# Kernel tuning notes

Measured on AMD Instinct MI355X. Metric: run time of the kernel, lower is better.

Reference implementation:

```python
import jax, jax.numpy as jnp
import numpy as np

EMBED_DIM = 256
NUM_HEADS = 8
HEAD_DIM = 32
INNER = NUM_HEADS * HEAD_DIM
NEG_SLOPE = 0.2


def setup_inputs() -> dict:
    key = jax.random.key(0)
    ks = jax.random.split(key, 8)
    B, Ns, Nt = 8, 1024, 1024
    src = jax.random.normal(ks[0], (B, Ns, EMBED_DIM), dtype=jnp.float32)
    trg = jax.random.normal(ks[1], (B, Nt, EMBED_DIM), dtype=jnp.float32)
    src_mask = jnp.ones((B, Ns), dtype=bool)
    trg_mask = jax.random.randint(ks[2], (B, Nt), 0, 2).astype(bool)
    # learned params (xavier-ish scale)
    def xavier(k, shape):
        fan_in, fan_out = shape[0], shape[-1]
        lim = (6.0 / (fan_in + fan_out)) ** 0.5
        return jax.random.uniform(k, shape, jnp.float32, -lim, lim)
    W_src = xavier(ks[3], (EMBED_DIM, INNER))
    W_trg = xavier(ks[4], (EMBED_DIM, INNER))  # is_cross_type=True -> independent
    a_src = xavier(ks[5], (NUM_HEADS, HEAD_DIM))
    a_trg = xavier(ks[6], (NUM_HEADS, HEAD_DIM))
    W_out = xavier(ks[7], (INNER, EMBED_DIM))
    return {"src": src, "trg": trg, "src_mask": src_mask, "trg_mask": trg_mask,
            "W_src": W_src, "W_trg": W_trg, "a_src": a_src, "a_trg": a_trg, "W_out": W_out}


def reference(src, trg, src_mask, trg_mask, W_src, W_trg, a_src, a_trg, W_out):
    B, Ns, _ = src.shape
    Nt = trg.shape[1]
    NH, Dh = NUM_HEADS, HEAD_DIM
    src_proj = (src @ W_src).reshape(B, Ns, NH, Dh)  # dropout p=0
    trg_proj = (trg @ W_trg).reshape(B, Nt, NH, Dh)
    score_src = jnp.einsum('bshd,hd->bsh', src_proj, a_src)
    score_trg = jnp.einsum('bthd,hd->bth', trg_proj, a_trg)
    # (B,Ns,NH,1) + (B,1,NH,Nt) -> (B,Ns,NH,Nt)
    scores = score_src[:, :, :, None] + jnp.transpose(score_trg, (0, 2, 1))[:, None, :, :]
    scores = jnp.where(scores >= 0, scores, NEG_SLOPE * scores)  # LeakyReLU
    edge_mask = src_mask[:, :, None, None] & trg_mask[:, None, None, :]
    scores = jnp.where(edge_mask, scores, -jnp.inf)
    attn = jax.nn.softmax(scores, axis=-1)
    attn = jnp.nan_to_num(attn, nan=0.0)
    aggregated = jnp.einsum('bsht,bthd->bshd', attn, trg_proj)
    output = aggregated.reshape(B, Ns, NH * Dh) @ W_out
    return output, jnp.transpose(attn, (0, 2, 1, 3))
```

## Files before the change

### kernel.cpp

```cpp
#include <hip/hip_runtime.h>
#include <hip/hip_bf16.h>
#include <math.h>

#define NB 8
#define NS 1024
#define NT 1024
#define NE 256
#define NHEADS 8
#define DH 32

typedef __attribute__((ext_vector_type(8))) short short8;
typedef __attribute__((ext_vector_type(8))) unsigned short ushort8;
typedef __attribute__((ext_vector_type(4))) float f32x4;

#define O_VT    0u
#define O_AGGB  (4u<<20)
#define O_WTT   (8u<<20)
#define O_WTO   ((8u<<20)+131072u)
#define O_CSRC  ((8u<<20)+262144u)
#define O_CTRG  (O_CSRC+8192u)
#define O_SSRC  (O_CTRG+8192u)
#define O_STRG  (O_SSRC+262144u)
#define O_FLAG  (O_STRG+262144u)

__device__ __forceinline__ unsigned short f2bf(float f) {
    __hip_bfloat16 h = __float2bfloat16(f);
    union { __hip_bfloat16 h; unsigned short u; } c; c.h = h;
    return c.u;
}
__device__ __forceinline__ float bf2f(unsigned short u) {
    union { unsigned u; float f; } x; x.u = ((unsigned)u) << 16;
    return x.f;
}
__device__ __forceinline__ float leaky(float v) {
    return (v >= 0.f) ? v : 0.2f * v;
}

__global__ __launch_bounds__(256) void setup_kernel(
    const unsigned* __restrict__ tmask_dw, const float* __restrict__ Wsrc,
    const float* __restrict__ Wtrg, const float* __restrict__ Wout,
    const float* __restrict__ asrc, const float* __restrict__ atrg,
    float* __restrict__ c_src, float* __restrict__ c_trg,
    unsigned short* __restrict__ Wt_t, unsigned short* __restrict__ Wt_o,
    int* __restrict__ flag) {
    __shared__ __align__(16) char sm[16640];
    const int tid = threadIdx.x;
    const int bid = blockIdx.x;

    if (bid == 0) {
        __shared__ int s_ok;
        if (tid == 0) s_ok = 1;
        __syncthreads();
        for (int i = tid; i < 2048; i += 256)
            if (tmask_dw[i] > 1u) s_ok = 0;
        __syncthreads();
        if (tid == 0) *flag = s_ok;
    } else if (bid <= 2) {
        float* a_sh = (float*)sm;
        const float* W = (bid == 1) ? Wsrc : Wtrg;
        const float* a = (bid == 1) ? asrc : atrg;
        float* c = (bid == 1) ? c_src : c_trg;
        a_sh[tid] = a[tid];
        __syncthreads();
        const int e = tid;
        float ch[8];
#pragma unroll
        for (int h = 0; h < 8; ++h) ch[h] = 0.f;
        for (int i = 0; i < 64; ++i) {
            const float4 wv = *(const float4*)&W[(size_t)e * NE + i * 4];
            const int h = i >> 3, d0 = (i & 7) * 4;
            ch[h] += wv.x * a_sh[h * 32 + d0] + wv.y * a_sh[h * 32 + d0 + 1] +
                     wv.z * a_sh[h * 32 + d0 + 2] + wv.w * a_sh[h * 32 + d0 + 3];
        }
#pragma unroll
        for (int h = 0; h < 8; ++h) c[h * NE + e] = ch[h];
    } else {
        const int q = bid - 3;
        const float* W = (q >> 4) ? Wout : Wtrg;
        unsigned short* Wt = (q >> 4) ? Wt_o : Wt_t;
        const int tl = q & 15;
        const int k0 = (tl >> 2) * 64, n0 = (tl & 3) * 64;
        float* xs = (float*)sm;
#pragma unroll
        for (int it = 0; it < 4; ++it) {
            const int slot = it * 256 + tid;
            const int k = slot >> 4, c4 = slot & 15;
            const float4 v = *(const float4*)&W[(size_t)(k0 + k) * NE + n0 + c4 * 4];
            float* p = &xs[k * 65 + c4 * 4];
            p[0] = v.x; p[1] = v.y; p[2] = v.z; p[3] = v.w;
        }
        __syncthreads();
#pragma unroll
        for (int it = 0; it < 2; ++it) {
            const int slot = it * 256 + tid;
            const int n = slot >> 3, kc = slot & 7;
            ushort8 v;
#pragma unroll
            for (int e = 0; e < 8; ++e)
                v[e] = f2bf(xs[(kc * 8 + e) * 65 + n]);
            *(ushort8*)&Wt[(size_t)(n0 + n) * NE + k0 + kc * 8] = v;
        }
    }
}

__global__ __launch_bounds__(256) void mid_kernel(
    const float* __restrict__ src, const float* __restrict__ trg,
    const float* __restrict__ c_src, const float* __restrict__ c_trg,
    const unsigned short* __restrict__ Wt_t, unsigned short* __restrict__ Vt,
    float* __restrict__ ssrc, float* __restrict__ strg) {
    __shared__ __align__(16) char sm[49152];
    const int tid = threadIdx.x;
    const int bid = blockIdx.x;

    if (bid < 256) {
        unsigned short* As = (unsigned short*)sm;
        unsigned short* ldsT = (unsigned short*)(sm + 32768);
        const int lane = tid & 63, w = tid >> 6;
        const int row0 = (bid >> 1) * 64;
        const int col0 = (bid & 1) * 128;

#pragma unroll
        for (int it = 0; it < 8; ++it) {
            const int gf = it * 256 + tid;
            const int row = gf >> 5, g3 = gf & 31;
            const float4 a = *(const float4*)&trg[(size_t)(row0 + row) * NE + g3 * 8];
            const float4 b = *(const float4*)&trg[(size_t)(row0 + row) * NE + g3 * 8 + 4];
            ushort8 v;
            v[0] = f2bf(a.x); v[1] = f2bf(a.y); v[2] = f2bf(a.z); v[3] = f2bf(a.w);
            v[4] = f2bf(b.x); v[5] = f2bf(b.y); v[6] = f2bf(b.z); v[7] = f2bf(b.w);
            *(ushort8*)&As[row * NE + ((g3 ^ (row & 7)) * 8)] = v;
        }
        __syncthreads();

        const int r = lane & 15, g = lane >> 4;
        short8 af[8];
#pragma unroll
        for (int kk = 0; kk < 8; ++kk)
            af[kk] = *(const short8*)&As[(w * 16 + r) * NE + (((kk * 4 + g) ^ (r & 7)) * 8)];

        f32x4 acc[8];
#pragma unroll
        for (int nt = 0; nt < 8; ++nt) acc[nt] = (f32x4){0.f, 0.f, 0.f, 0.f};
#pragma unroll
        for (int kk = 0; kk < 8; ++kk) {
#pragma unroll
            for (int nt = 0; nt < 8; ++nt) {
                const int col = col0 + nt * 16 + r;
                const short8 bf = *(const short8*)&Wt_t[(size_t)col * NE + kk * 32 + g * 8];
                acc[nt] = __builtin_amdgcn_mfma_f32_16x16x32_bf16(af[kk], bf, acc[nt], 0, 0, 0);
            }
        }
        __syncthreads();

#pragma unroll
        for (int nt = 0; nt < 8; ++nt) {
            const int cl = nt * 16 + r;
            const int sw = (cl & 7) << 3;
#pragma unroll
            for (int j = 0; j < 4; ++j) {
                const int t = w * 16 + g * 4 + j;
                ldsT[cl * 64 + (t ^ sw)] = f2bf(acc[nt][j]);
            }
        }
        __syncthreads();

        const int b = row0 >> 10, t0 = row0 & 1023;
#pragma unroll
        for (int it = 0; it < 4; ++it) {
            const int slot = it * 256 + tid;
            const int cl = slot >> 3, ch = slot & 7;
            const int colg = col0 + cl;
            const int h = colg >> 5, d = colg & 31;
            *(ushort8*)&Vt[(((size_t)(b * 8 + h)) * 32 + d) * 1024 + t0 + ch * 8] =
                *(const ushort8*)&ldsT[cl * 64 + ch * 8];
        }
    } else {
        float* xs = (float*)sm;
        float* cs = (float*)(sm + 32768);
        const int rowg0 = (bid - 256) * 32;
        const bool is_src = rowg0 < NB * NS;
        const float* X = is_src ? (src + (size_t)rowg0 * NE)
                                : (trg + (size_t)(rowg0 - NB * NS) * NE);
        const float* C = is_src ? c_src : c_trg;
        float* S = is_src ? (ssrc + (size_t)rowg0 * NHEADS)
                          : (strg + (size_t)(rowg0 - NB * NS) * NHEADS);

#pragma unroll
        for (int it = 0; it < 8; ++it) {
            const int slot = it * 256 + tid;
            const int row = slot >> 6, c4 = slot & 63;
            *(float4*)&xs[row * NE + c4 * 4] =
                *(const float4*)&X[(size_t)row * NE + c4 * 4];
            cs[slot] = C[slot];
        }
        __syncthreads();

        const int r = tid >> 3, h = tid & 7;
        float s = 0.f;
        for (int e = 0; e < NE; e += 4) {
            const float4 x = *(const float4*)&xs[r * NE + e];
            const float4 c = *(const float4*)&cs[h * NE + e];
            s += x.x * c.x + x.y * c.y + x.z * c.z + x.w * c.w;
        }
        S[(size_t)r * NHEADS + h] = s;
    }
}

__global__ __launch_bounds__(256) void fused_softmax_agg_kernel(
    const float* __restrict__ ssrc, const float* __restrict__ strg,
    const void* __restrict__ smask, const void* __restrict__ tmask,
    const int* __restrict__ flag_p, const unsigned short* __restrict__ Vt,
    float* __restrict__ attn, unsigned short* __restrict__ agg_bf) {
    const int blk = blockIdx.x;
    const int stile = blk & 15;
    const int h = (blk >> 4) & 7;
    const int b = blk >> 7;
    const int tid = threadIdx.x;
    const int lane = tid & 63;
    const int wave = tid >> 6;
    const int flag = *flag_p;

    __shared__ __align__(16) float s_sm[NT];
    __shared__ float s_inv[64];
    __shared__ float s_ss[64];

    for (int t = tid; t < NT; t += 256) {
        const bool mv = flag ? (((const int*)tmask)[b * NT + t] != 0)
                             : (((const unsigned char*)tmask)[b * NT + t] != 0);
        s_sm[t] = mv ? strg[((size_t)b * NT + t) * NHEADS + h] : -1e30f;
    }
    __syncthreads();

    const int r = lane & 15;
    const int g = lane >> 4;
    const int srow = stile * 64 + wave * 16 + r;
    const float ss = ssrc[((size_t)b * NS + srow) * NHEADS + h];
    const bool rowv = flag ? (((const int*)smask)[b * NS + srow] != 0)
                           : (((const unsigned char*)smask)[b * NS + srow] != 0);
    const int sw = (r & 7) << 3;
    const unsigned short* vr0 = Vt + (size_t)(b * NHEADS + h) * 32768 + r * 1024;
    const unsigned short* vr1 = vr0 + 16 * 1024;

    f32x4 acc0 = {0.f, 0.f, 0.f, 0.f};
    f32x4 acc1 = {0.f, 0.f, 0.f, 0.f};
    float sum = 0.f;
#pragma unroll 4
    for (int c = 0; c < 32; ++c) {
        const int tb = c * 32 + g * 8;
        const short8 b0 = *(const short8*)&vr0[tb ^ sw];
        const short8 b1 = *(const short8*)&vr1[tb ^ sw];
        const float4 v0 = *(const float4*)&s_sm[tb];
        const float4 v1 = *(const float4*)&s_sm[tb + 4];
        const float vv[8] = {v0.x, v0.y, v0.z, v0.w, v1.x, v1.y, v1.z, v1.w};
        short8 pa;
#pragma unroll
        for (int e = 0; e < 8; ++e) {
            const float p = __expf(leaky(ss + vv[e]));
            sum += p;
            pa[e] = (short)f2bf(p);
        }
        acc0 = __builtin_amdgcn_mfma_f32_16x16x32_bf16(pa, b0, acc0, 0, 0, 0);
        acc1 = __builtin_amdgcn_mfma_f32_16x16x32_bf16(pa, b1, acc1, 0, 0, 0);
    }

    sum += __shfl_xor(sum, 16);
    sum += __shfl_xor(sum, 32);
    const float inv = (rowv && sum > 0.f) ? 1.f / sum : 0.f;
    if (g == 0) {
        s_inv[wave * 16 + r] = inv;
        s_ss[wave * 16 + r] = ss;
    }
    __syncthreads();

    {
        const int orow = stile * 64 + wave * 16 + g * 4;
        unsigned short* ab = agg_bf + ((size_t)b * NS + orow) * NE + h * DH + r;
#pragma unroll
        for (int j = 0; j < 4; ++j) {
            const float iv = s_inv[wave * 16 + g * 4 + j];
            ab[(size_t)j * NE] = f2bf(acc0[j] * iv);
            ab[(size_t)j * NE + 16] = f2bf(acc1[j] * iv);
        }
    }

    float* wbase = attn + ((size_t)((b * NHEADS + h) * NS) + stile * 64 + wave * 16) * NT;
    const float* ssv = &s_ss[wave * 16];
    const float* invv = &s_inv[wave * 16];
    for (int rr = 0; rr < 16; ++rr) {
        const float ssr = ssv[rr];
        const float ivr = invv[rr];
        float* arow = wbase + (size_t)rr * NT;
#pragma unroll
        for (int q = 0; q < 4; ++q) {
            const int t0 = q * 256 + lane * 4;
            const float4 sm4 = *(const float4*)&s_sm[t0];
            float4 o;
            o.x = __expf(leaky(ssr + sm4.x)) * ivr;
            o.y = __expf(leaky(ssr + sm4.y)) * ivr;
            o.z = __expf(leaky(ssr + sm4.z)) * ivr;
            o.w = __expf(leaky(ssr + sm4.w)) * ivr;
            *(float4*)&arow[t0] = o;
        }
    }
}

__global__ __launch_bounds__(256) void gemm_out_kernel(
    const unsigned short* __restrict__ Xb, const unsigned short* __restrict__ Wt,
    float* __restrict__ Yf) {
    __shared__ __align__(16) unsigned short As[64 * NE];
    const int tid = threadIdx.x;
    const int lane = tid & 63;
    const int w = tid >> 6;
    const int row0 = blockIdx.x * 64;
    const int col0 = blockIdx.y * 128;

#pragma unroll
    for (int it = 0; it < 8; ++it) {
        const int gf = it * 256 + tid;
        const int row = gf >> 5, g3 = gf & 31;
        const ushort8 v = *(const ushort8*)&Xb[(size_t)(row0 + row) * NE + g3 * 8];
        *(ushort8*)&As[row * NE + ((g3 ^ (row & 7)) * 8)] = v;
    }
    __syncthreads();

    const int r = lane & 15, g = lane >> 4;
    short8 af[8];
#pragma unroll
    for (int kk = 0; kk < 8; ++kk)
        af[kk] = *(const short8*)&As[(w * 16 + r) * NE + (((kk * 4 + g) ^ (r & 7)) * 8)];

    f32x4 acc[8];
#pragma unroll
    for (int nt = 0; nt < 8; ++nt) acc[nt] = (f32x4){0.f, 0.f, 0.f, 0.f};
#pragma unroll
    for (int kk = 0; kk < 8; ++kk) {
#pragma unroll
        for (int nt = 0; nt < 8; ++nt) {
            const int col = col0 + nt * 16 + r;
            const short8 bf = *(const short8*)&Wt[(size_t)col * NE + kk * 32 + g * 8];
            acc[nt] = __builtin_amdgcn_mfma_f32_16x16x32_bf16(af[kk], bf, acc[nt], 0, 0, 0);
        }
    }

#pragma unroll
    for (int nt = 0; nt < 8; ++nt) {
        const int col = col0 + nt * 16 + r;
#pragma unroll
        for (int j = 0; j < 4; ++j) {
            const int row = row0 + w * 16 + g * 4 + j;
            Yf[(size_t)row * NE + col] = acc[nt][j];
        }
    }
}

extern "C" void kernel_launch(void* const* d_in, const int* in_sizes, int n_in,
                              void* d_out, int out_size, void* d_ws, size_t ws_size,
                              hipStream_t stream) {
    const float* src   = (const float*)d_in[0];
    const float* trg   = (const float*)d_in[1];
    const void*  smask = d_in[2];
    const void*  tmask = d_in[3];
    const float* Wsrc  = (const float*)d_in[4];
    const float* Wtrg  = (const float*)d_in[5];
    const float* asrc  = (const float*)d_in[6];
    const float* atrg  = (const float*)d_in[7];
    const float* Wout  = (const float*)d_in[8];

    float* out  = (float*)d_out;
    float* attn = out + (size_t)NB * NS * NE;

    char* wsb = (char*)d_ws;
    unsigned short* Vt     = (unsigned short*)(wsb + O_VT);
    unsigned short* agg_bf = (unsigned short*)(wsb + O_AGGB);
    unsigned short* Wt_t   = (unsigned short*)(wsb + O_WTT);
    unsigned short* Wt_o   = (unsigned short*)(wsb + O_WTO);
    float* c_src = (float*)(wsb + O_CSRC);
    float* c_trg = (float*)(wsb + O_CTRG);
    float* ssrc  = (float*)(wsb + O_SSRC);
    float* strg  = (float*)(wsb + O_STRG);
    int*   flag  = (int*)(wsb + O_FLAG);

    setup_kernel<<<35, 256, 0, stream>>>(
        (const unsigned*)tmask, Wsrc, Wtrg, Wout, asrc, atrg,
        c_src, c_trg, Wt_t, Wt_o, flag);

    mid_kernel<<<768, 256, 0, stream>>>(
        src, trg, c_src, c_trg, Wt_t, Vt, ssrc, strg);

    fused_softmax_agg_kernel<<<NB * NHEADS * (NS / 64), 256, 0, stream>>>(
        ssrc, strg, smask, tmask, flag, Vt, attn, agg_bf);

    gemm_out_kernel<<<dim3(128, 2), 256, 0, stream>>>(agg_bf, Wt_o, out);
}
```

Measured before the change: 98.49 us.

## Fuse output projection into softmax-aggregation kernel with all heads per block

Each block now handles a 16-row source tile across all eight heads, with each wave covering two heads. The aggregated tile stays in swizzled shared memory and the W_out GEMM runs in the same kernel. This removes the separate gemm_out launch and the bf16 aggregate round trip through global memory. Softmax exponentials become raw v_exp_f32 on log2e-prescaled scores. In exchange, shared memory grows to about 40KB per block, the grid shrinks to 512 blocks, and each block repeats the W_out reads.

Result: no change. 98.16 us (-0.3%).

```diff
diff --git a/kernel.cpp b/kernel.cpp
--- a/kernel.cpp
+++ b/kernel.cpp
@@ -8,13 +8,13 @@
 #define NE 256
 #define NHEADS 8
 #define DH 32
+#define LOG2E 1.4426950408889634f
 
 typedef __attribute__((ext_vector_type(8))) short short8;
 typedef __attribute__((ext_vector_type(8))) unsigned short ushort8;
 typedef __attribute__((ext_vector_type(4))) float f32x4;
 
 #define O_VT    0u
-#define O_AGGB  (4u<<20)
 #define O_WTT   (8u<<20)
 #define O_WTO   ((8u<<20)+131072u)
 #define O_CSRC  ((8u<<20)+262144u)
@@ -28,12 +28,13 @@
     union { __hip_bfloat16 h; unsigned short u; } c; c.h = h;
     return c.u;
 }
-__device__ __forceinline__ float bf2f(unsigned short u) {
-    union { unsigned u; float f; } x; x.u = ((unsigned)u) << 16;
-    return x.f;
-}
 __device__ __forceinline__ float leaky(float v) {
     return (v >= 0.f) ? v : 0.2f * v;
+}
+__device__ __forceinline__ float exp2_fast(float x) {
+    float r;
+    asm("v_exp_f32 %0, %1" : "=v"(r) : "v"(x));
+    return r;
 }
 
 __global__ __launch_bounds__(256) void setup_kernel(
@@ -206,149 +207,139 @@
     }
 }
 
-__global__ __launch_bounds__(256) void fused_softmax_agg_kernel(
+__global__ __launch_bounds__(256) void fused_kernel(
     const float* __restrict__ ssrc, const float* __restrict__ strg,
     const void* __restrict__ smask, const void* __restrict__ tmask,
     const int* __restrict__ flag_p, const unsigned short* __restrict__ Vt,
-    float* __restrict__ attn, unsigned short* __restrict__ agg_bf) {
+    const unsigned short* __restrict__ Wt_o,
+    float* __restrict__ attn, float* __restrict__ out) {
     const int blk = blockIdx.x;
-    const int stile = blk & 15;
-    const int h = (blk >> 4) & 7;
-    const int b = blk >> 7;
+    const int q = blk & 63;
+    const int b = blk >> 6;
     const int tid = threadIdx.x;
     const int lane = tid & 63;
-    const int wave = tid >> 6;
+    const int w = tid >> 6;
     const int flag = *flag_p;
 
-    __shared__ __align__(16) float s_sm[NT];
-    __shared__ float s_inv[64];
-    __shared__ float s_ss[64];
+    __shared__ __align__(16) float s_sm[8][1024];
+    __shared__ __align__(16) unsigned short agg_sw[16 * 256];
+    __shared__ float s_inv[8][16];
+    __shared__ float s_ssv[8][16];
 
     for (int t = tid; t < NT; t += 256) {
         const bool mv = flag ? (((const int*)tmask)[b * NT + t] != 0)
                              : (((const unsigned char*)tmask)[b * NT + t] != 0);
-        s_sm[t] = mv ? strg[((size_t)b * NT + t) * NHEADS + h] : -1e30f;
+        const float4 s0 = *(const float4*)&strg[((size_t)b * NT + t) * 8];
+        const float4 s1 = *(const float4*)&strg[((size_t)b * NT + t) * 8 + 4];
+        const float sv[8] = {s0.x, s0.y, s0.z, s0.w, s1.x, s1.y, s1.z, s1.w};
+#pragma unroll
+        for (int h = 0; h < 8; ++h)
+            s_sm[h][t] = mv ? sv[h] * LOG2E : -1e30f;
     }
     __syncthreads();
 
     const int r = lane & 15;
     const int g = lane >> 4;
-    const int srow = stile * 64 + wave * 16 + r;
-    const float ss = ssrc[((size_t)b * NS + srow) * NHEADS + h];
+    const int srow = q * 16 + r;
     const bool rowv = flag ? (((const int*)smask)[b * NS + srow] != 0)
                            : (((const unsigned char*)smask)[b * NS + srow] != 0);
     const int sw = (r & 7) << 3;
-    const unsigned short* vr0 = Vt + (size_t)(b * NHEADS + h) * 32768 + r * 1024;
-    const unsigned short* vr1 = vr0 + 16 * 1024;
-
-    f32x4 acc0 = {0.f, 0.f, 0.f, 0.f};
-    f32x4 acc1 = {0.f, 0.f, 0.f, 0.f};
-    float sum = 0.f;
+
+    f32x4 acc0[2], acc1[2];
+
+#pragma unroll
+    for (int hh = 0; hh < 2; ++hh) {
+        const int h = w * 2 + hh;
+        const float ss2 = ssrc[((size_t)b * NS + srow) * NHEADS + h] * LOG2E;
+        const unsigned short* vr0 = Vt + (size_t)(b * 8 + h) * 32768 + r * 1024;
+        const unsigned short* vr1 = vr0 + 16 * 1024;
+        f32x4 a0 = {0.f, 0.f, 0.f, 0.f};
+        f32x4 a1 = {0.f, 0.f, 0.f, 0.f};
+        float sum = 0.f;
 #pragma unroll 4
-    for (int c = 0; c < 32; ++c) {
-        const int tb = c * 32 + g * 8;
-        const short8 b0 = *(const short8*)&vr0[tb ^ sw];
-        const short8 b1 = *(const short8*)&vr1[tb ^ sw];
-        const float4 v0 = *(const float4*)&s_sm[tb];
-        const float4 v1 = *(const float4*)&s_sm[tb + 4];
-        const float vv[8] = {v0.x, v0.y, v0.z, v0.w, v1.x, v1.y, v1.z, v1.w};
-        short8 pa;
-#pragma unroll
-        for (int e = 0; e < 8; ++e) {
-            const float p = __expf(leaky(ss + vv[e]));
-            sum += p;
-            pa[e] = (short)f2bf(p);
-        }
-        acc0 = __builtin_amdgcn_mfma_f32_16x16x32_bf16(pa, b0, acc0, 0, 0, 0);
-        acc1 = __builtin_amdgcn_mfma_f32_16x16x32_bf16(pa, b1, acc1, 0, 0, 0);
-    }
-
-    sum += __shfl_xor(sum, 16);
-    sum += __shfl_xor(sum, 32);
-    const float inv = (rowv && sum > 0.f) ? 1.f / sum : 0.f;
-    if (g == 0) {
-        s_inv[wave * 16 + r] = inv;
-        s_ss[wave * 16 + r] = ss;
+        for (int c = 0; c < 32; ++c) {
+            const int tb = c * 32 + g * 8;
+            const short8 b0 = *(const short8*)&vr0[tb ^ sw];
+            const short8 b1 = *(const short8*)&vr1[tb ^ sw];
+            const float4 v0 = *(const float4*)&s_sm[h][tb];
+            const float4 v1 = *(const float4*)&s_sm[h][tb + 4];
+            const float vv[8] = {v0.x, v0.y, v0.z, v0.w, v1.x, v1.y, v1.z, v1.w};
+            short8 pa;
+#pragma unroll
+            for (int e = 0; e < 8; ++e) {
+                const float p = exp2_fast(leaky(ss2 + vv[e]));
+                sum += p;
+                pa[e] = (short)f2bf(p);
+            }
+            a0 = __builtin_amdgcn_mfma_f32_16x16x32_bf16(pa, b0, a0, 0, 0, 0);
+            a1 = __builtin_amdgcn_mfma_f32_16x16x32_bf16(pa, b1, a1, 0, 0, 0);
+        }
+        sum += __shfl_xor(sum, 16);
+        sum += __shfl_xor(sum, 32);
+        const float inv = (rowv && sum > 0.f) ? 1.f / sum : 0.f;
+        if (g == 0) {
+            s_inv[h][r] = inv;
+            s_ssv[h][r] = ss2;
+        }
+        acc0[hh] = a0;
+        acc1[hh] = a1;
     }
     __syncthreads();
 
-    {
-        const int orow = stile * 64 + wave * 16 + g * 4;
-        unsigned short* ab = agg_bf + ((size_t)b * NS + orow) * NE + h * DH + r;
+#pragma unroll
+    for (int hh = 0; hh < 2; ++hh) {
+        const int h = w * 2 + hh;
 #pragma unroll
         for (int j = 0; j < 4; ++j) {
-            const float iv = s_inv[wave * 16 + g * 4 + j];
-            ab[(size_t)j * NE] = f2bf(acc0[j] * iv);
-            ab[(size_t)j * NE + 16] = f2bf(acc1[j] * iv);
-        }
-    }
-
-    float* wbase = attn + ((size_t)((b * NHEADS + h) * NS) + stile * 64 + wave * 16) * NT;
-    const float* ssv = &s_ss[wave * 16];
-    const float* invv = &s_inv[wave * 16];
-    for (int rr = 0; rr < 16; ++rr) {
-        const float ssr = ssv[rr];
-        const float ivr = invv[rr];
-        float* arow = wbase + (size_t)rr * NT;
-#pragma unroll
-        for (int q = 0; q < 4; ++q) {
-            const int t0 = q * 256 + lane * 4;
-            const float4 sm4 = *(const float4*)&s_sm[t0];
+            const int row = g * 4 + j;
+            const float iv = s_inv[h][row];
+            int col = h * 32 + r;
+            agg_sw[row * 256 + ((((col >> 3) ^ (row & 7)) << 3) | (col & 7))] =
+                f2bf(acc0[hh][j] * iv);
+            col += 16;
+            agg_sw[row * 256 + ((((col >> 3) ^ (row & 7)) << 3) | (col & 7))] =
+                f2bf(acc1[hh][j] * iv);
+        }
+    }
+    __syncthreads();
+
+    f32x4 oacc[4];
+#pragma unroll
+    for (int nt = 0; nt < 4; ++nt) oacc[nt] = (f32x4){0.f, 0.f, 0.f, 0.f};
+#pragma unroll
+    for (int kk = 0; kk < 8; ++kk) {
+        const short8 af = *(const short8*)&agg_sw[r * 256 + (((kk * 4 + g) ^ (r & 7)) * 8)];
+#pragma unroll
+        for (int nt = 0; nt < 4; ++nt) {
+            const int col = w * 64 + nt * 16 + r;
+            const short8 bf = *(const short8*)&Wt_o[(size_t)col * NE + kk * 32 + g * 8];
+            oacc[nt] = __builtin_amdgcn_mfma_f32_16x16x32_bf16(af, bf, oacc[nt], 0, 0, 0);
+        }
+    }
+#pragma unroll
+    for (int nt = 0; nt < 4; ++nt) {
+        const int col = w * 64 + nt * 16 + r;
+#pragma unroll
+        for (int j = 0; j < 4; ++j)
+            out[((size_t)b * NS + q * 16 + g * 4 + j) * NE + col] = oacc[nt][j];
+    }
+
+    for (int i = 0; i < 32; ++i) {
+        const int idx = w * 32 + i;
+        const int h = idx >> 4, rr = idx & 15;
+        const float ssr = s_ssv[h][rr];
+        const float ivr = s_inv[h][rr];
+        float* arow = attn + ((size_t)(b * NHEADS + h) * NS + q * 16 + rr) * NT;
+#pragma unroll
+        for (int qq = 0; qq < 4; ++qq) {
+            const int t0 = qq * 256 + lane * 4;
+            const float4 sm4 = *(const float4*)&s_sm[h][t0];
             float4 o;
-            o.x = __expf(leaky(ssr + sm4.x)) * ivr;
-            o.y = __expf(leaky(ssr + sm4.y)) * ivr;
-            o.z = __expf(leaky(ssr + sm4.z)) * ivr;
-            o.w = __expf(leaky(ssr + sm4.w)) * ivr;
+            o.x = exp2_fast(leaky(ssr + sm4.x)) * ivr;
+            o.y = exp2_fast(leaky(ssr + sm4.y)) * ivr;
+            o.z = exp2_fast(leaky(ssr + sm4.z)) * ivr;
+            o.w = exp2_fast(leaky(ssr + sm4.w)) * ivr;
             *(float4*)&arow[t0] = o;
-        }
-    }
-}
-
-__global__ __launch_bounds__(256) void gemm_out_kernel(
-    const unsigned short* __restrict__ Xb, const unsigned short* __restrict__ Wt,
-    float* __restrict__ Yf) {
-    __shared__ __align__(16) unsigned short As[64 * NE];
-    const int tid = threadIdx.x;
-    const int lane = tid & 63;
-    const int w = tid >> 6;
-    const int row0 = blockIdx.x * 64;
-    const int col0 = blockIdx.y * 128;
-
-#pragma unroll
-    for (int it = 0; it < 8; ++it) {
-        const int gf = it * 256 + tid;
-        const int row = gf >> 5, g3 = gf & 31;
-        const ushort8 v = *(const ushort8*)&Xb[(size_t)(row0 + row) * NE + g3 * 8];
-        *(ushort8*)&As[row * NE + ((g3 ^ (row & 7)) * 8)] = v;
-    }
-    __syncthreads();
-
-    const int r = lane & 15, g = lane >> 4;
-    short8 af[8];
-#pragma unroll
-    for (int kk = 0; kk < 8; ++kk)
-        af[kk] = *(const short8*)&As[(w * 16 + r) * NE + (((kk * 4 + g) ^ (r & 7)) * 8)];
-
-    f32x4 acc[8];
-#pragma unroll
-    for (int nt = 0; nt < 8; ++nt) acc[nt] = (f32x4){0.f, 0.f, 0.f, 0.f};
-#pragma unroll
-    for (int kk = 0; kk < 8; ++kk) {
-#pragma unroll
-        for (int nt = 0; nt < 8; ++nt) {
-            const int col = col0 + nt * 16 + r;
-            const short8 bf = *(const short8*)&Wt[(size_t)col * NE + kk * 32 + g * 8];
-            acc[nt] = __builtin_amdgcn_mfma_f32_16x16x32_bf16(af[kk], bf, acc[nt], 0, 0, 0);
-        }
-    }
-
-#pragma unroll
-    for (int nt = 0; nt < 8; ++nt) {
-        const int col = col0 + nt * 16 + r;
-#pragma unroll
-        for (int j = 0; j < 4; ++j) {
-            const int row = row0 + w * 16 + g * 4 + j;
-            Yf[(size_t)row * NE + col] = acc[nt][j];
         }
     }
 }
@@ -370,10 +361,9 @@
     float* attn = out + (size_t)NB * NS * NE;
 
     char* wsb = (char*)d_ws;
-    unsigned short* Vt     = (unsigned short*)(wsb + O_VT);
-    unsigned short* agg_bf = (unsigned short*)(wsb + O_AGGB);
-    unsigned short* Wt_t   = (unsigned short*)(wsb + O_WTT);
-    unsigned short* Wt_o   = (unsigned short*)(wsb + O_WTO);
+    unsigned short* Vt   = (unsigned short*)(wsb + O_VT);
+    unsigned short* Wt_t = (unsigned short*)(wsb + O_WTT);
+    unsigned short* Wt_o = (unsigned short*)(wsb + O_WTO);
     float* c_src = (float*)(wsb + O_CSRC);
     float* c_trg = (float*)(wsb + O_CTRG);
     float* ssrc  = (float*)(wsb + O_SSRC);
@@ -387,8 +377,6 @@
     mid_kernel<<<768, 256, 0, stream>>>(
         src, trg, c_src, c_trg, Wt_t, Vt, ssrc, strg);
 
-    fused_softmax_agg_kernel<<<NB * NHEADS * (NS / 64), 256, 0, stream>>>(
-        ssrc, strg, smask, tmask, flag, Vt, attn, agg_bf);
-
-    gemm_out_kernel<<<dim3(128, 2), 256, 0, stream>>>(agg_bf, Wt_o, out);
-}
+    fused_kernel<<<NB * (NS / 16), 256, 0, stream>>>(
+        ssrc, strg, smask, tmask, flag, Vt, Wt_o, attn, out);
+}
```
